# Kernel tuning notes

Measured on AMD Instinct MI355X. Metric: run time of the kernel, lower is better.

The kernel has to match this reference:

```python
import jax, jax.numpy as jnp
import numpy as np

VOLRADIUS = 64.0
DT = 1.0 / VOLRADIUS          # normalized step size (dt / volradius)
NSTEPS = 64                   # covers t in [0, 1.0) at step DT


def setup_inputs() -> dict:
    key = jax.random.key(0)
    ks = jax.random.split(key, 8)
    B, H, W, K, M = 1, 128, 128, 32, 16
    # ray origins near volume center, unit directions
    raypos = 0.2 * jax.random.normal(ks[0], (B, H, W, 3), jnp.float32)
    rd = jax.random.normal(ks[1], (B, H, W, 3), jnp.float32)
    raydir = rd / jnp.linalg.norm(rd, axis=-1, keepdims=True)
    tmin = jnp.zeros((B, H, W), jnp.float32)
    tmax = 0.9 + 0.1 * jax.random.uniform(ks[2], (B, H, W), dtype=jnp.float32)
    tminmax = jnp.stack([tmin, tmax], axis=-1)
    # primitive poses: positions, rotations (orthonormal via QR), inverse-scales
    primpos = 0.3 * jax.random.normal(ks[3], (B, K, 3), jnp.float32)
    A = jax.random.normal(ks[4], (B, K, 3, 3), jnp.float32)
    primrot, _ = jnp.linalg.qr(A)
    primscale = 1.0 + 2.0 * jax.random.uniform(ks[5], (B, K, 3), dtype=jnp.float32)
    # RGBA voxel payload per primitive; alpha channel nonnegative (decoder emits nonneg density)
    template = jax.random.normal(ks[6], (B, K, 4, M, M, M), jnp.float32)
    template = template.at[:, :, 3].set(2.0 * jax.nn.softplus(template[:, :, 3]))
    return dict(raypos=raypos, raydir=raydir, tminmax=tminmax, primpos=primpos,
                primrot=primrot, primscale=primscale, template=template)


def _trilinear(template, y):
    # template [B,K,C,M,M,M]; y [B,R,K,3] normalized coords in [-1,1] (align_corners)
    B, K, C, M = template.shape[0], template.shape[1], template.shape[2], template.shape[3]
    g = (y + 1.0) * 0.5 * (M - 1)
    i0 = jnp.clip(jnp.floor(g), 0, M - 2).astype(jnp.int32)
    f = jnp.clip(g - i0.astype(g.dtype), 0.0, 1.0)
    i1 = i0 + 1
    bidx = jnp.arange(B)[:, None, None]
    kidx = jnp.arange(K)[None, None, :]

    def corner(iz, iy, ix):
        # advanced-index gather -> [B,R,K,C]
        return template[bidx, kidx, :, iz, iy, ix]

    fz, fy, fx = f[..., 0:1], f[..., 1:2], f[..., 2:3]
    i0z, i0y, i0x = i0[..., 0], i0[..., 1], i0[..., 2]
    i1z, i1y, i1x = i1[..., 0], i1[..., 1], i1[..., 2]
    v = ((1 - fz) * (1 - fy) * (1 - fx) * corner(i0z, i0y, i0x)
         + (1 - fz) * (1 - fy) * fx * corner(i0z, i0y, i1x)
         + (1 - fz) * fy * (1 - fx) * corner(i0z, i1y, i0x)
         + (1 - fz) * fy * fx * corner(i0z, i1y, i1x)
         + fz * (1 - fy) * (1 - fx) * corner(i1z, i0y, i0x)
         + fz * (1 - fy) * fx * corner(i1z, i0y, i1x)
         + fz * fy * (1 - fx) * corner(i1z, i1y, i0x)
         + fz * fy * fx * corner(i1z, i1y, i1x))
    return v  # [B,R,K,C]


def reference(raypos, raydir, tminmax, primpos, primrot, primscale, template):
    B, H, W, _ = raypos.shape
    R = H * W
    rp = raypos.reshape(B, R, 3)
    rd = raydir.reshape(B, R, 3)
    tmm = tminmax.reshape(B, R, 2)
    tmin, tmax = tmm[..., 0:1], tmm[..., 1:2]

    def step(carry, i):
        rgb, alpha = carry
        t = tmin + i * DT                                   # [B,R,1]
        pos = rp + rd * t                                   # [B,R,3]
        xl = pos[:, :, None, :] - primpos[:, None, :, :]    # [B,R,K,3]
        yloc = jnp.einsum('bkij,brkj->brki', primrot, xl) * primscale[:, None, :, :]
        inside = jnp.all(jnp.abs(yloc) <= 1.0, axis=-1, keepdims=True).astype(rgb.dtype)
        samp = (_trilinear(template, yloc) * inside).sum(axis=2)   # [B,R,4]
        srgb, salpha = samp[..., :3], samp[..., 3:4]
        valid = (t < tmax).astype(rgb.dtype)
        # clamped additive compositing (Neural Volumes / MVP)
        newalpha = jnp.clip(alpha + salpha * DT * valid, 0.0, 1.0)
        contrib = newalpha - alpha
        return (rgb + srgb * contrib, newalpha), None

    init = (jnp.zeros((B, R, 3), raypos.dtype), jnp.zeros((B, R, 1), raypos.dtype))
    (rgb, alpha), _ = jax.lax.scan(step, init, jnp.arange(NSTEPS, dtype=raypos.dtype))

    rayrgba = jnp.concatenate([rgb, alpha], axis=-1).reshape(B, H, W, 4)
    rayrgba = jnp.transpose(rayrgba, (0, 3, 1, 2))   # [B,4,H,W]
    rayrgb = rayrgba[:, :3]
    rayalpha = rayrgba[:, 3:4]
    return rayrgb, rayalpha, rayrgba
```

## Files before the change

### kernel.cpp

```cpp
#include <hip/hip_runtime.h>
#include <hip/hip_fp16.h>


namespace {

constexpr float kDT  = 1.0f / 64.0f;
constexpr int   kVox = 32 * 4096;

struct H4 { __half2 lo, hi; };

__global__ __launch_bounds__(256) void transpose_tmpl_h(
    const float* __restrict__ tmpl, H4* __restrict__ wsH)
{
    const int idx = blockIdx.x * 256 + threadIdx.x;
    const int k   = idx >> 12;
    const int rem = idx & 4095;
    const float* src = tmpl + k * 16384 + rem;
    H4 v;
    v.lo = __floats2half2_rn(src[0],    src[4096]);
    v.hi = __floats2half2_rn(src[8192], src[12288]);
    wsH[idx] = v;
}

__device__ __forceinline__ __half2 lerp2(__half2 a, __half2 b, __half2 f) {
    return __hfma2(f, __hsub2(b, a), a);
}

__global__ __launch_bounds__(256) void raymarch8(
    const float* __restrict__ raypos,
    const float* __restrict__ raydir,
    const float* __restrict__ tminmax,
    const float* __restrict__ primpos,
    const float* __restrict__ primrot,
    const float* __restrict__ primscale,
    const H4* __restrict__ wsH,
    float* __restrict__ out,
    int R)
{
    const int lane = threadIdx.x & 63;
    const int wid  = threadIdx.x >> 6;
    const int k    = lane & 31;
    const int half = lane >> 5;
    const int ray  = blockIdx.x * 8 + wid * 2 + half;

    const float rpx = raypos[ray * 3 + 0];
    const float rpy = raypos[ray * 3 + 1];
    const float rpz = raypos[ray * 3 + 2];
    const float rdx = raydir[ray * 3 + 0];
    const float rdy = raydir[ray * 3 + 1];
    const float rdz = raydir[ray * 3 + 2];
    const float tmin = tminmax[ray * 2 + 0];
    const float tmax = tminmax[ray * 2 + 1];

    float A0, A1, A2, D0, D1, D2;
    {
        const float ox = rpx - primpos[k * 3 + 0];
        const float oy = rpy - primpos[k * 3 + 1];
        const float oz = rpz - primpos[k * 3 + 2];
        const float s0 = primscale[k * 3 + 0];
        const float s1 = primscale[k * 3 + 1];
        const float s2 = primscale[k * 3 + 2];
        const float* rk = primrot + k * 9;
        A0 = (rk[0] * ox + rk[1] * oy + rk[2] * oz) * s0;
        D0 = (rk[0] * rdx + rk[1] * rdy + rk[2] * rdz) * s0;
        A1 = (rk[3] * ox + rk[4] * oy + rk[5] * oz) * s1;
        D1 = (rk[3] * rdx + rk[4] * rdy + rk[5] * rdz) * s1;
        A2 = (rk[6] * ox + rk[7] * oy + rk[8] * oz) * s2;
        D2 = (rk[6] * rdx + rk[7] * rdy + rk[8] * rdz) * s2;
    }

    const H4* __restrict__ tbase = wsH + k * 4096;

    float alpha = 0.f;
    float r0 = 0.f, r1 = 0.f, r2 = 0.f;

    for (int i = 0; i < 64; ++i) {
        const float t = fmaf((float)i, kDT, tmin);
        const bool live = (t < tmax) && (alpha < 1.0f);
        if (__ballot(live) == 0ull) break;

        const float y0 = fmaf(D0, t, A0);
        const float y1 = fmaf(D1, t, A1);
        const float y2 = fmaf(D2, t, A2);
        const bool inside = live && fabsf(y0) <= 1.0f && fabsf(y1) <= 1.0f
                                 && fabsf(y2) <= 1.0f;
        if (__ballot(inside) == 0ull) continue;

        float s0 = 0.f, s1 = 0.f, s2 = 0.f, s3 = 0.f;
        if (inside) {
            const float gz = fmaf(y0, 7.5f, 7.5f);
            const float gy = fmaf(y1, 7.5f, 7.5f);
            const float gx = fmaf(y2, 7.5f, 7.5f);
            const int iz = min((int)gz, 14);
            const int iy = min((int)gy, 14);
            const int ix = min((int)gx, 14);
            const float fz = fminf(gz - (float)iz, 1.0f);
            const float fy = fminf(gy - (float)iy, 1.0f);
            const float fx = fminf(gx - (float)ix, 1.0f);

            const H4* tp = tbase + (iz * 256 + iy * 16 + ix);
            const H4 c000 = tp[0];
            const H4 c001 = tp[1];
            const H4 c010 = tp[16];
            const H4 c011 = tp[17];
            const H4 c100 = tp[256];
            const H4 c101 = tp[257];
            const H4 c110 = tp[272];
            const H4 c111 = tp[273];

            const __half2 hz = __float2half2_rn(fz);
            const __half2 hy = __float2half2_rn(fy);
            const __half2 hx = __float2half2_rn(fx);

            const __half2 m00l = lerp2(c000.lo, c100.lo, hz);
            const __half2 m00h = lerp2(c000.hi, c100.hi, hz);
            const __half2 m01l = lerp2(c001.lo, c101.lo, hz);
            const __half2 m01h = lerp2(c001.hi, c101.hi, hz);
            const __half2 m10l = lerp2(c010.lo, c110.lo, hz);
            const __half2 m10h = lerp2(c010.hi, c110.hi, hz);
            const __half2 m11l = lerp2(c011.lo, c111.lo, hz);
            const __half2 m11h = lerp2(c011.hi, c111.hi, hz);

            const __half2 n0l = lerp2(m00l, m10l, hy);
            const __half2 n0h = lerp2(m00h, m10h, hy);
            const __half2 n1l = lerp2(m01l, m11l, hy);
            const __half2 n1h = lerp2(m01h, m11h, hy);

            const __half2 vl = lerp2(n0l, n1l, hx);
            const __half2 vh = lerp2(n0h, n1h, hx);

            const float2 fLo = __half22float2(vl);
            const float2 fHi = __half22float2(vh);
            s0 = fLo.x; s1 = fLo.y; s2 = fHi.x; s3 = fHi.y;
        }

        float tot3 = s3;
        #pragma unroll
        for (int m = 1; m < 32; m <<= 1) tot3 += __shfl_xor(tot3, m);

        const float na = fminf(fmaf(tot3, kDT, alpha), 1.0f);
        const float contrib = na - alpha;
        alpha = na;
        r0 = fmaf(s0, contrib, r0);
        r1 = fmaf(s1, contrib, r1);
        r2 = fmaf(s2, contrib, r2);
    }

    #pragma unroll
    for (int m = 1; m < 32; m <<= 1) {
        r0 += __shfl_xor(r0, m);
        r1 += __shfl_xor(r1, m);
        r2 += __shfl_xor(r2, m);
    }

    if (k == 0) {
        out[0 * R + ray] = r0;
        out[1 * R + ray] = r1;
        out[2 * R + ray] = r2;
        out[3 * R + ray] = alpha;
        out[4 * R + ray] = r0;
        out[5 * R + ray] = r1;
        out[6 * R + ray] = r2;
        out[7 * R + ray] = alpha;
    }
}

__global__ __launch_bounds__(256) void raymarch_fb(
    const float* __restrict__ raypos, const float* __restrict__ raydir,
    const float* __restrict__ tminmax, const float* __restrict__ primpos,
    const float* __restrict__ primrot, const float* __restrict__ primscale,
    const float* __restrict__ tmpl, float* __restrict__ out, int R)
{
    const int lane = threadIdx.x & 63;
    const int wid  = threadIdx.x >> 6;
    const int k    = lane & 31;
    const int half = lane >> 5;
    const int ray  = blockIdx.x * 8 + wid * 2 + half;

    const float rpx = raypos[ray*3+0], rpy = raypos[ray*3+1], rpz = raypos[ray*3+2];
    const float rdx = raydir[ray*3+0], rdy = raydir[ray*3+1], rdz = raydir[ray*3+2];
    const float tmin = tminmax[ray*2+0], tmax = tminmax[ray*2+1];

    float A0,A1,A2,D0,D1,D2;
    {
        const float ox = rpx - primpos[k*3+0], oy = rpy - primpos[k*3+1], oz = rpz - primpos[k*3+2];
        const float s0 = primscale[k*3+0], s1 = primscale[k*3+1], s2 = primscale[k*3+2];
        const float* rk = primrot + k*9;
        A0 = (rk[0]*ox+rk[1]*oy+rk[2]*oz)*s0; D0 = (rk[0]*rdx+rk[1]*rdy+rk[2]*rdz)*s0;
        A1 = (rk[3]*ox+rk[4]*oy+rk[5]*oz)*s1; D1 = (rk[3]*rdx+rk[4]*rdy+rk[5]*rdz)*s1;
        A2 = (rk[6]*ox+rk[7]*oy+rk[8]*oz)*s2; D2 = (rk[6]*rdx+rk[7]*rdy+rk[8]*rdz)*s2;
    }
    float alpha = 0.f, r0 = 0.f, r1 = 0.f, r2 = 0.f;
    for (int i = 0; i < 64; ++i) {
        const float t = fmaf((float)i, kDT, tmin);
        const bool live = (t < tmax) && (alpha < 1.0f);
        if (__ballot(live) == 0ull) break;
        const float y0 = fmaf(D0,t,A0), y1 = fmaf(D1,t,A1), y2 = fmaf(D2,t,A2);
        const bool inside = live && fabsf(y0)<=1.f && fabsf(y1)<=1.f && fabsf(y2)<=1.f;
        if (__ballot(inside) == 0ull) continue;
        float s0=0.f,s1=0.f,s2=0.f,s3=0.f;
        if (inside) {
            const float gz=(y0+1.f)*7.5f, gy=(y1+1.f)*7.5f, gx=(y2+1.f)*7.5f;
            const int iz=(int)fminf(floorf(gz),14.f), iy=(int)fminf(floorf(gy),14.f), ix=(int)fminf(floorf(gx),14.f);
            const float fz=fminf(gz-(float)iz,1.f), fy=fminf(gy-(float)iy,1.f), fx=fminf(gx-(float)ix,1.f);
            const float oz_=1.f-fz, oy_=1.f-fy, ox_=1.f-fx;
            const float w000=oz_*oy_*ox_, w001=oz_*oy_*fx, w010=oz_*fy*ox_, w011=oz_*fy*fx;
            const float w100=fz*oy_*ox_, w101=fz*oy_*fx, w110=fz*fy*ox_, w111=fz*fy*fx;
            const float* tp = tmpl + k*16384 + iz*256 + iy*16 + ix;
            float acc[4];
            #pragma unroll
            for (int c = 0; c < 4; ++c) {
                const float* tc = tp + c*4096;
                acc[c] = w000*tc[0]+w001*tc[1]+w010*tc[16]+w011*tc[17]
                       + w100*tc[256]+w101*tc[257]+w110*tc[272]+w111*tc[273];
            }
            s0=acc[0]; s1=acc[1]; s2=acc[2]; s3=acc[3];
        }
        float tot3 = s3;
        #pragma unroll
        for (int m = 1; m < 32; m <<= 1) tot3 += __shfl_xor(tot3, m);
        const float na = fminf(fmaf(tot3, kDT, alpha), 1.0f);
        const float contrib = na - alpha;
        alpha = na;
        r0 = fmaf(s0, contrib, r0); r1 = fmaf(s1, contrib, r1); r2 = fmaf(s2, contrib, r2);
    }
    #pragma unroll
    for (int m = 1; m < 32; m <<= 1) {
        r0 += __shfl_xor(r0, m); r1 += __shfl_xor(r1, m); r2 += __shfl_xor(r2, m);
    }
    if (k == 0) {
        out[0*R+ray]=r0; out[1*R+ray]=r1; out[2*R+ray]=r2; out[3*R+ray]=alpha;
        out[4*R+ray]=r0; out[5*R+ray]=r1; out[6*R+ray]=r2; out[7*R+ray]=alpha;
    }
}

}

extern "C" void kernel_launch(void* const* d_in, const int* in_sizes, int n_in,
                              void* d_out, int out_size, void* d_ws, size_t ws_size,
                              hipStream_t stream) {
    const float* raypos    = (const float*)d_in[0];
    const float* raydir    = (const float*)d_in[1];
    const float* tminmax   = (const float*)d_in[2];
    const float* primpos   = (const float*)d_in[3];
    const float* primrot   = (const float*)d_in[4];
    const float* primscale = (const float*)d_in[5];
    const float* tmpl      = (const float*)d_in[6];
    float* out = (float*)d_out;

    const int R = in_sizes[0] / 3;
    const size_t needH = (size_t)kVox * sizeof(H4);

    if (ws_size >= needH) {
        H4* wsH = (H4*)d_ws;
        transpose_tmpl_h<<<dim3(kVox / 256), dim3(256), 0, stream>>>(tmpl, wsH);
        raymarch8<<<dim3(R / 8), dim3(256), 0, stream>>>(
            raypos, raydir, tminmax, primpos, primrot, primscale, wsH, out, R);
    } else {
        raymarch_fb<<<dim3(R / 8), dim3(256), 0, stream>>>(
            raypos, raydir, tminmax, primpos, primrot, primscale, tmpl, out, R);
    }
}
```

Baseline: 97.15 us.

## Assign one ray per wavefront, splitting alternate march steps across half-waves

Each 64-lane wavefront now handles a single ray. The two 32-lane halves evaluate even and odd march steps in parallel, and the pair is composited in order using a cross-half shuffle. This cuts the sequential loop to 32 iterations, so per-ray latency and divergent early-exit waste should drop, at the cost of twice as many wavefronts overall. The eight corner loads are merged into four 16-byte paired loads. Those paired loads assume 8-byte alignment that odd voxel indices may not give, and alpha clamping between the paired steps must stay exact.

After: 89.09 us. -8.3%, faster.

```diff
diff --git a/kernel.cpp b/kernel.cpp
--- a/kernel.cpp
+++ b/kernel.cpp
@@ -8,6 +8,7 @@
 constexpr int   kVox = 32 * 4096;
 
 struct H4 { __half2 lo, hi; };
+struct __attribute__((aligned(8))) H4x2 { __half2 l0, h0, l1, h1; };
 
 __global__ __launch_bounds__(256) void transpose_tmpl_h(
     const float* __restrict__ tmpl, H4* __restrict__ wsH)
@@ -26,7 +27,7 @@
     return __hfma2(f, __hsub2(b, a), a);
 }
 
-__global__ __launch_bounds__(256) void raymarch8(
+__global__ __launch_bounds__(256) void raymarch9(
     const float* __restrict__ raypos,
     const float* __restrict__ raydir,
     const float* __restrict__ tminmax,
@@ -37,11 +38,11 @@
     float* __restrict__ out,
     int R)
 {
-    const int lane = threadIdx.x & 63;
-    const int wid  = threadIdx.x >> 6;
-    const int k    = lane & 31;
-    const int half = lane >> 5;
-    const int ray  = blockIdx.x * 8 + wid * 2 + half;
+    const int lane   = threadIdx.x & 63;
+    const int wid    = threadIdx.x >> 6;
+    const int k      = lane & 31;
+    const int parity = lane >> 5;
+    const int ray    = blockIdx.x * 4 + wid;
 
     const float rpx = raypos[ray * 3 + 0];
     const float rpy = raypos[ray * 3 + 1];
@@ -74,16 +75,16 @@
     float alpha = 0.f;
     float r0 = 0.f, r1 = 0.f, r2 = 0.f;
 
-    for (int i = 0; i < 64; ++i) {
-        const float t = fmaf((float)i, kDT, tmin);
-        const bool live = (t < tmax) && (alpha < 1.0f);
-        if (__ballot(live) == 0ull) break;
-
-        const float y0 = fmaf(D0, t, A0);
-        const float y1 = fmaf(D1, t, A1);
-        const float y2 = fmaf(D2, t, A2);
-        const bool inside = live && fabsf(y0) <= 1.0f && fabsf(y1) <= 1.0f
-                                 && fabsf(y2) <= 1.0f;
+    for (int j = 0; j < 32; ++j) {
+        const float t0 = fmaf((float)(2 * j), kDT, tmin);
+        if (t0 >= tmax || alpha >= 1.0f) break;
+
+        const float tl = fmaf((float)(2 * j + parity), kDT, tmin);
+        const float y0 = fmaf(D0, tl, A0);
+        const float y1 = fmaf(D1, tl, A1);
+        const float y2 = fmaf(D2, tl, A2);
+        const bool inside = (tl < tmax) && fabsf(y0) <= 1.0f
+                         && fabsf(y1) <= 1.0f && fabsf(y2) <= 1.0f;
         if (__ballot(inside) == 0ull) continue;
 
         float s0 = 0.f, s1 = 0.f, s2 = 0.f, s3 = 0.f;
@@ -99,61 +100,67 @@
             const float fx = fminf(gx - (float)ix, 1.0f);
 
             const H4* tp = tbase + (iz * 256 + iy * 16 + ix);
-            const H4 c000 = tp[0];
-            const H4 c001 = tp[1];
-            const H4 c010 = tp[16];
-            const H4 c011 = tp[17];
-            const H4 c100 = tp[256];
-            const H4 c101 = tp[257];
-            const H4 c110 = tp[272];
-            const H4 c111 = tp[273];
+            const H4x2 p00 = *(const H4x2*)(tp + 0);
+            const H4x2 p01 = *(const H4x2*)(tp + 16);
+            const H4x2 p10 = *(const H4x2*)(tp + 256);
+            const H4x2 p11 = *(const H4x2*)(tp + 272);
 
             const __half2 hz = __float2half2_rn(fz);
             const __half2 hy = __float2half2_rn(fy);
             const __half2 hx = __float2half2_rn(fx);
 
-            const __half2 m00l = lerp2(c000.lo, c100.lo, hz);
-            const __half2 m00h = lerp2(c000.hi, c100.hi, hz);
-            const __half2 m01l = lerp2(c001.lo, c101.lo, hz);
-            const __half2 m01h = lerp2(c001.hi, c101.hi, hz);
-            const __half2 m10l = lerp2(c010.lo, c110.lo, hz);
-            const __half2 m10h = lerp2(c010.hi, c110.hi, hz);
-            const __half2 m11l = lerp2(c011.lo, c111.lo, hz);
-            const __half2 m11h = lerp2(c011.hi, c111.hi, hz);
-
-            const __half2 n0l = lerp2(m00l, m10l, hy);
-            const __half2 n0h = lerp2(m00h, m10h, hy);
-            const __half2 n1l = lerp2(m01l, m11l, hy);
-            const __half2 n1h = lerp2(m01h, m11h, hy);
-
-            const __half2 vl = lerp2(n0l, n1l, hx);
-            const __half2 vh = lerp2(n0h, n1h, hx);
+            const __half2 q0l0 = lerp2(p00.l0, p10.l0, hz);
+            const __half2 q0h0 = lerp2(p00.h0, p10.h0, hz);
+            const __half2 q0l1 = lerp2(p00.l1, p10.l1, hz);
+            const __half2 q0h1 = lerp2(p00.h1, p10.h1, hz);
+            const __half2 q1l0 = lerp2(p01.l0, p11.l0, hz);
+            const __half2 q1h0 = lerp2(p01.h0, p11.h0, hz);
+            const __half2 q1l1 = lerp2(p01.l1, p11.l1, hz);
+            const __half2 q1h1 = lerp2(p01.h1, p11.h1, hz);
+
+            const __half2 ul0 = lerp2(q0l0, q1l0, hy);
+            const __half2 uh0 = lerp2(q0h0, q1h0, hy);
+            const __half2 ul1 = lerp2(q0l1, q1l1, hy);
+            const __half2 uh1 = lerp2(q0h1, q1h1, hy);
+
+            const __half2 vl = lerp2(ul0, ul1, hx);
+            const __half2 vh = lerp2(uh0, uh1, hx);
 
             const float2 fLo = __half22float2(vl);
             const float2 fHi = __half22float2(vh);
             s0 = fLo.x; s1 = fLo.y; s2 = fHi.x; s3 = fHi.y;
         }
 
-        float tot3 = s3;
+        float tot = s3;
         #pragma unroll
-        for (int m = 1; m < 32; m <<= 1) tot3 += __shfl_xor(tot3, m);
-
-        const float na = fminf(fmaf(tot3, kDT, alpha), 1.0f);
-        const float contrib = na - alpha;
-        alpha = na;
+        for (int m = 1; m < 32; m <<= 1) tot += __shfl_xor(tot, m);
+        const float other = __shfl_xor(tot, 32);
+        const float te = parity ? other : tot;
+        const float to = parity ? tot : other;
+
+        const float t1v = fmaf((float)(2 * j + 1), kDT, tmin);
+        const float a_e = te * kDT;
+        const float a_o = (t1v < tmax) ? to * kDT : 0.0f;
+        const float na1 = fminf(alpha + a_e, 1.0f);
+        const float c_e = na1 - alpha;
+        const float na2 = fminf(na1 + a_o, 1.0f);
+        const float c_o = na2 - na1;
+        alpha = na2;
+
+        const float contrib = parity ? c_o : c_e;
         r0 = fmaf(s0, contrib, r0);
         r1 = fmaf(s1, contrib, r1);
         r2 = fmaf(s2, contrib, r2);
     }
 
     #pragma unroll
-    for (int m = 1; m < 32; m <<= 1) {
+    for (int m = 1; m < 64; m <<= 1) {
         r0 += __shfl_xor(r0, m);
         r1 += __shfl_xor(r1, m);
         r2 += __shfl_xor(r2, m);
     }
 
-    if (k == 0) {
+    if (lane == 0) {
         out[0 * R + ray] = r0;
         out[1 * R + ray] = r1;
         out[2 * R + ray] = r2;
@@ -254,7 +261,7 @@
     if (ws_size >= needH) {
         H4* wsH = (H4*)d_ws;
         transpose_tmpl_h<<<dim3(kVox / 256), dim3(256), 0, stream>>>(tmpl, wsH);
-        raymarch8<<<dim3(R / 8), dim3(256), 0, stream>>>(
+        raymarch9<<<dim3(R / 4), dim3(256), 0, stream>>>(
             raypos, raydir, tminmax, primpos, primrot, primscale, wsH, out, R);
     } else {
         raymarch_fb<<<dim3(R / 8), dim3(256), 0, stream>>>(
```
